# Optimization experiments

Hardware: AMD Instinct MI355X
Metric: run time of the kernel (lower is better)

The kernel has to match this reference:

```python
import jax, jax.numpy as jnp
import numpy as np

IN_DIMS = 256
EMBED_DIMS = 512
NUM_HEADS = 8
GRID = 16  # forced: arrange2 hardcodes 256 = GRID*GRID tokens
HEAD_DIM = EMBED_DIMS // NUM_HEADS
LN_EPS = 1e-5


def setup_inputs() -> dict:
    key = jax.random.key(0)
    ks = jax.random.split(key, 12)
    B = 8
    s_in = 1.0 / np.sqrt(IN_DIMS)
    s_emb = 1.0 / np.sqrt(EMBED_DIMS)
    return {
        "x1": jax.random.normal(ks[0], (B, IN_DIMS, GRID, GRID), jnp.float32),
        "x2": jax.random.normal(ks[1], (B, IN_DIMS, GRID, GRID), jnp.float32),
        # 1x1 conv weights stored as [out, in]
        "Wq": jax.random.normal(ks[2], (EMBED_DIMS, IN_DIMS), jnp.float32) * s_in,
        "bq": jnp.zeros((EMBED_DIMS,), jnp.float32),
        "Wk": jax.random.normal(ks[3], (EMBED_DIMS, IN_DIMS), jnp.float32) * s_in,
        "bk": jnp.zeros((EMBED_DIMS,), jnp.float32),
        "Wv": jax.random.normal(ks[4], (EMBED_DIMS, IN_DIMS), jnp.float32) * s_in,
        "bv": jnp.zeros((EMBED_DIMS,), jnp.float32),
        "Wa": jax.random.normal(ks[5], (IN_DIMS, EMBED_DIMS), jnp.float32) * s_emb,
        "ba": jnp.zeros((IN_DIMS,), jnp.float32),
        "ln_g": jnp.ones((IN_DIMS,), jnp.float32),
        "ln_b": jnp.zeros((IN_DIMS,), jnp.float32),
        "Wl": jax.random.normal(ks[6], (IN_DIMS, IN_DIMS), jnp.float32) * s_in,
        "bl": jnp.zeros((IN_DIMS,), jnp.float32),
    }


def _conv1x1(x, W, b):
    # x: [b, Cin, h, w]; W: [Cout, Cin]
    return jnp.einsum('bihw,oi->bohw', x, W) + b[None, :, None, None]


def _arrange(t):
    # 'b (c head) h w -> head b (h w) c'  (c outer, head inner in channel axis)
    b = t.shape[0]
    t = t.reshape(b, HEAD_DIM, NUM_HEADS, GRID * GRID)
    return t.transpose(2, 0, 3, 1)  # [head, b, n, c]


def reference(x1, x2, Wq, bq, Wk, bk, Wv, bv, Wa, ba, ln_g, ln_b, Wl, bl):
    B, Cin, H, W = x1.shape
    N = H * W  # 256
    q = _arrange(_conv1x1(x1, Wq, bq))                     # [h, b, n, c]
    k = _arrange(_conv1x1(x2, Wk, bk))                     # [h, q, m, c]
    v = _arrange(_conv1x1(x2, Wv, bv)).reshape(NUM_HEADS, B * N, HEAD_DIM)  # [h, (b m), c]
    # cross-batch attention logits (NOTE: original never applies self.scale)
    attn = jnp.einsum('pbnc,pqmc->pbqnm', q, k)            # [h, b, q, n, m]
    attn = jax.nn.softmax(attn, axis=-1)
    # 'head b q n m -> b head n (q m)'
    attn = attn.transpose(1, 0, 3, 2, 4).reshape(B, NUM_HEADS, N, B * N)
    out = jnp.einsum('bhnm,hmc->bhnc', attn, v)            # [b, h, n, c]
    # 'b head (h w) c -> b (c head) h w'
    out = out.transpose(0, 3, 1, 2).reshape(B, EMBED_DIMS, H, W)
    a = _conv1x1(out, Wa, ba) + x1                          # residual, [b, Cin, h, w]
    # proj_out: rearrange -> LayerNorm -> Linear -> ReLU -> rearrange back
    t = a.reshape(B, Cin, N).transpose(0, 2, 1)            # [b, n, Cin]
    mu = t.mean(-1, keepdims=True)
    var = ((t - mu) ** 2).mean(-1, keepdims=True)
    t = (t - mu) * jax.lax.rsqrt(var + LN_EPS) * ln_g + ln_b
    t = jax.nn.relu(t @ Wl.T + bl)
    return t.transpose(0, 2, 1).reshape(B, Cin, H, W)
```

## Files before the change

### kernel.cpp

```cpp
#include <hip/hip_runtime.h>

typedef unsigned short u16;
typedef unsigned int   u32;
typedef __attribute__((ext_vector_type(8))) short bf16x8;
typedef __attribute__((ext_vector_type(4))) float f32x4;

#define BB   8
#define CIN  256
#define NT   256
#define EMB  512
#define NH   8

__device__ __forceinline__ float bf2f(u16 b) {
    union { u32 u; float f; } v; v.u = ((u32)b) << 16; return v.f;
}
__device__ __forceinline__ u16 f2bf(float f) {
    union { float f; u32 u; } v; v.f = f;
    u32 r = v.u + 0x7FFFu + ((v.u >> 16) & 1u);
    return (u16)(r >> 16);
}
__device__ __forceinline__ float ld(const u16* base, size_t idx, int f32) {
    return f32 ? ((const float*)base)[idx] : bf2f(base[idx]);
}

struct alignas(16) U32x4 { u32 x, y, z, w; };
struct alignas(8)  U32x2 { u32 x, y; };

__global__ void k_xpose(
    const u16* __restrict__ x1, const u16* __restrict__ x2,
    const u16* __restrict__ Wq, const u16* __restrict__ Wk, const u16* __restrict__ Wv,
    u16* __restrict__ XTh, u16* __restrict__ XTl,
    u16* __restrict__ WCh, u16* __restrict__ WCl,
    int* __restrict__ flag)
{
    __shared__ int cnt;
    __shared__ float T[64][65];
    int t = threadIdx.x;
    if (t == 0) cnt = 0;
    __syncthreads();
    {
        int local = 0;
        for (int j = t * 16; j < t * 16 + 16; j += 2) {
            u16 w = x1[j];
            int e = (w >> 7) & 0xFF;
            if (e >= 100 && e <= 145) local++;
        }
        atomicAdd(&cnt, local);
    }
    __syncthreads();
    const int f32 = (cnt >= 1200) ? 0 : 1;

    int bid = blockIdx.x;
    if (bid == 0 && t == 0) *flag = f32;

    if (bid < 256) {
        int inp = bid >> 7, b = (bid >> 4) & 7, ks = (bid >> 2) & 3, ns = bid & 3;
        const u16* X = inp ? x2 : x1;
#pragma unroll
        for (int p = 0; p < 4; ++p) {
            int kk = p * 16 + (t >> 4);
            int nn = (t & 15) * 4;
#pragma unroll
            for (int j = 0; j < 4; ++j)
                T[kk][nn + j] = ld(X, ((size_t)b * CIN + ks * 64 + kk) * NT + ns * 64 + nn + j, f32);
        }
        __syncthreads();
#pragma unroll
        for (int it = 0; it < 2; ++it) {
            int g = it * 256 + t;
            int nn = g >> 3, kg = g & 7;
            u32 hw[4], lw[4];
#pragma unroll
            for (int e = 0; e < 4; ++e) {
                float va = T[kg * 8 + 2 * e][nn];
                float vb = T[kg * 8 + 2 * e + 1][nn];
                u16 ha = f2bf(va), hb = f2bf(vb);
                u16 la = f2bf(va - bf2f(ha)), lb = f2bf(vb - bf2f(hb));
                hw[e] = (u32)ha | ((u32)hb << 16);
                lw[e] = (u32)la | ((u32)lb << 16);
            }
            size_t dst = (((size_t)(inp * 8 + b) * 256) + ns * 64 + nn) * 256 + ks * 64 + kg * 8;
            U32x4 H; H.x = hw[0]; H.y = hw[1]; H.z = hw[2]; H.w = hw[3];
            U32x4 L; L.x = lw[0]; L.y = lw[1]; L.z = lw[2]; L.w = lw[3];
            *(U32x4*)&XTh[dst] = H;
            *(U32x4*)&XTl[dst] = L;
        }
    } else {
        int wb = bid - 256;
        int proj = wb >> 2, qtr = wb & 3;
        const u16* W = (proj == 0) ? Wq : (proj == 1) ? Wk : Wv;
#pragma unroll
        for (int it = 0; it < 16; ++it) {
            int g = it * 256 + t;
            int row = g >> 5, kg = g & 31;
            int o = qtr * 128 + row;
            u32 hw[4], lw[4];
#pragma unroll
            for (int e = 0; e < 4; ++e) {
                float va = ld(W, (size_t)o * CIN + kg * 8 + 2 * e, f32);
                float vb = ld(W, (size_t)o * CIN + kg * 8 + 2 * e + 1, f32);
                u16 ha = f2bf(va), hb = f2bf(vb);
                u16 la = f2bf(va - bf2f(ha)), lb = f2bf(vb - bf2f(hb));
                hw[e] = (u32)ha | ((u32)hb << 16);
                lw[e] = (u32)la | ((u32)lb << 16);
            }
            size_t dst = ((size_t)(proj * 512 + o)) * 256 + kg * 8;
            U32x4 H; H.x = hw[0]; H.y = hw[1]; H.z = hw[2]; H.w = hw[3];
            U32x4 L; L.x = lw[0]; L.y = lw[1]; L.z = lw[2]; L.w = lw[3];
            *(U32x4*)&WCh[dst] = H;
            *(U32x4*)&WCl[dst] = L;
        }
    }
}

__global__ __launch_bounds__(256) void k_qkv(
    const u16* __restrict__ XTh, const u16* __restrict__ XTl,
    const u16* __restrict__ WCh, const u16* __restrict__ WCl,
    const u16* __restrict__ bq, const u16* __restrict__ bk, const u16* __restrict__ bv,
    u16* __restrict__ Qg, u16* __restrict__ Kg, u16* __restrict__ Vg,
    const int* __restrict__ flag)
{
    const int f32 = *flag;
    int id = blockIdx.x;
    int proj = id >> 8;
    int rem  = id & 255;
    int b  = rem >> 5;
    int ot = (rem >> 2) & 7;
    int nt = rem & 3;

    __shared__ __align__(16) u16 SB[16384];
    const int WHO = 0, WLO = 4096, XHO = 8192, XLO = 12288;

    int t = threadIdx.x;
    int l = t & 63, w = t >> 6;
    int quad = l >> 4, col = l & 15;
    const int lswz2 = l ^ (((l >> 4) & 1) << 1);

    const u16* Wh  = WCh + ((size_t)proj * 512 + ot * 64) * 256;
    const u16* Wlo = WCl + ((size_t)proj * 512 + ot * 64) * 256;
    int inp = (proj == 0) ? 0 : 1;
    const u16* Xh  = XTh + (((size_t)(inp * 8 + b)) * 256 + nt * 64) * 256;
    const u16* Xlo = XTl + (((size_t)(inp * 8 + b)) * 256 + nt * 64) * 256;

    f32x4 acc[4];
#pragma unroll
    for (int n4 = 0; n4 < 4; ++n4) { acc[n4][0]=0.f; acc[n4][1]=0.f; acc[n4][2]=0.f; acc[n4][3]=0.f; }

    for (int c4 = 0; c4 < 4; ++c4) {
        __syncthreads();
#pragma unroll
        for (int it = 0; it < 2; ++it) {
            int g = it * 256 + t;
            int row = g >> 3, cc = g & 7;
            int tt = row >> 4, klo = row & 15, kch = cc >> 2, qs = cc & 3;
            int pos = qs * 16 + (klo ^ ((qs & 1) << 1) ^ (kch << 2));
            int off = ((tt * 2 + kch) * 64 + pos) * 8;
            size_t src = (size_t)row * 256 + c4 * 64 + cc * 8;
            *(U32x4*)&SB[WHO + off] = *(const U32x4*)&Wh[src];
            *(U32x4*)&SB[WLO + off] = *(const U32x4*)&Wlo[src];
            *(U32x4*)&SB[XHO + off] = *(const U32x4*)&Xh[src];
            *(U32x4*)&SB[XLO + off] = *(const U32x4*)&Xlo[src];
        }
        __syncthreads();

        int sA0 = ((w * 2 + 0) * 64 + lswz2) * 8;
        int sA1 = ((w * 2 + 1) * 64 + (lswz2 ^ 4)) * 8;
        bf16x8 aH0 = *(const bf16x8*)&SB[WHO + sA0];
        bf16x8 aH1 = *(const bf16x8*)&SB[WHO + sA1];
        bf16x8 aL0 = *(const bf16x8*)&SB[WLO + sA0];
        bf16x8 aL1 = *(const bf16x8*)&SB[WLO + sA1];
#pragma unroll
        for (int n4 = 0; n4 < 4; ++n4) {
            int sB0 = ((n4 * 2 + 0) * 64 + lswz2) * 8;
            int sB1 = ((n4 * 2 + 1) * 64 + (lswz2 ^ 4)) * 8;
            bf16x8 bH0 = *(const bf16x8*)&SB[XHO + sB0];
            bf16x8 bH1 = *(const bf16x8*)&SB[XHO + sB1];
            bf16x8 bL0 = *(const bf16x8*)&SB[XLO + sB0];
            bf16x8 bL1 = *(const bf16x8*)&SB[XLO + sB1];
            acc[n4] = __builtin_amdgcn_mfma_f32_16x16x32_bf16(aH0, bH0, acc[n4], 0, 0, 0);
            acc[n4] = __builtin_amdgcn_mfma_f32_16x16x32_bf16(aH1, bH1, acc[n4], 0, 0, 0);
            acc[n4] = __builtin_amdgcn_mfma_f32_16x16x32_bf16(aL0, bH0, acc[n4], 0, 0, 0);
            acc[n4] = __builtin_amdgcn_mfma_f32_16x16x32_bf16(aL1, bH1, acc[n4], 0, 0, 0);
            acc[n4] = __builtin_amdgcn_mfma_f32_16x16x32_bf16(aH0, bL0, acc[n4], 0, 0, 0);
            acc[n4] = __builtin_amdgcn_mfma_f32_16x16x32_bf16(aH1, bL1, acc[n4], 0, 0, 0);
        }
    }
    __syncthreads();

    float (*EP)[68] = (float (*)[68])SB;
    const u16* bias = (proj == 0) ? bq : (proj == 1) ? bk : bv;
#pragma unroll
    for (int r = 0; r < 4; ++r) {
        int ol = w * 16 + quad * 4 + r;
        float bb = ld(bias, ot * 64 + ol, f32);
#pragma unroll
        for (int n4 = 0; n4 < 4; ++n4)
            EP[ol][n4 * 16 + col] = acc[n4][r] + bb;
    }
    __syncthreads();

    if (proj < 2) {
        u16* OUT = (proj == 0) ? Qg : Kg;
        int hh = t >> 5;
        int nb = t & 31;
#pragma unroll
        for (int p = 0; p < 2; ++p) {
            int nn = nb + 32 * p;
            u32 pk[4];
#pragma unroll
            for (int e = 0; e < 4; ++e) {
                u16 lo = f2bf(EP[(2 * e) * 8 + hh][nn]);
                u16 hi = f2bf(EP[(2 * e + 1) * 8 + hh][nn]);
                pk[e] = (u32)lo | ((u32)hi << 16);
            }
            U32x4 v; v.x = pk[0]; v.y = pk[1]; v.z = pk[2]; v.w = pk[3];
            *(U32x4*)&OUT[((size_t)((hh * 8 + b) * 256) + nt * 64 + nn) * 64 + ot * 8] = v;
        }
    } else {
        int rr = t >> 2;
        int hh = rr & 7, cl = rr >> 3;
        int nq = t & 3;
        u32 pk[8];
#pragma unroll
        for (int e = 0; e < 8; ++e) {
            u16 lo = f2bf(EP[cl * 8 + hh][nq * 16 + 2 * e]);
            u16 hi = f2bf(EP[cl * 8 + hh][nq * 16 + 2 * e + 1]);
            pk[e] = (u32)lo | ((u32)hi << 16);
        }
        size_t base = ((size_t)((hh * 8 + b) * 64) + ot * 8 + cl) * 256 + nt * 64 + nq * 16;
        U32x4 v0; v0.x = pk[0]; v0.y = pk[1]; v0.z = pk[2]; v0.w = pk[3];
        U32x4 v1; v1.x = pk[4]; v1.y = pk[5]; v1.z = pk[6]; v1.w = pk[7];
        *(U32x4*)&Vg[base]     = v0;
        *(U32x4*)&Vg[base + 8] = v1;
    }
}

__device__ __forceinline__ void softmax_p(f32x4 (&Sfr)[16], bf16x8 (&pf)[8]) {
    float inv;
    {
        float m = Sfr[0][0];
#pragma unroll
        for (int tt = 0; tt < 16; ++tt)
#pragma unroll
            for (int r = 0; r < 4; ++r) m = fmaxf(m, Sfr[tt][r]);
        m = fmaxf(m, __shfl_xor(m, 16));
        m = fmaxf(m, __shfl_xor(m, 32));
        float s = 0.f;
#pragma unroll
        for (int tt = 0; tt < 16; ++tt)
#pragma unroll
            for (int r = 0; r < 4; ++r) {
                float e = __expf(Sfr[tt][r] - m);
                Sfr[tt][r] = e; s += e;
            }
        s += __shfl_xor(s, 16);
        s += __shfl_xor(s, 32);
        inv = 1.f / s;
    }
#pragma unroll
    for (int ch = 0; ch < 8; ++ch) {
        float a0 = Sfr[2*ch  ][0]*inv, a1 = Sfr[2*ch  ][1]*inv;
        float a2 = Sfr[2*ch  ][2]*inv, a3 = Sfr[2*ch  ][3]*inv;
        float b0 = Sfr[2*ch+1][0]*inv, b1 = Sfr[2*ch+1][1]*inv;
        float b2 = Sfr[2*ch+1][2]*inv, b3 = Sfr[2*ch+1][3]*inv;
        u32 u0, u1, v0, v1;
        asm("v_cvt_pk_bf16_f32 %0, %1, %2" : "=v"(u0) : "v"(a0), "v"(a1));
        asm("v_cvt_pk_bf16_f32 %0, %1, %2" : "=v"(u1) : "v"(a2), "v"(a3));
        asm("v_cvt_pk_bf16_f32 %0, %1, %2" : "=v"(v0) : "v"(b0), "v"(b1));
        asm("v_cvt_pk_bf16_f32 %0, %1, %2" : "=v"(v1) : "v"(b2), "v"(b3));
        asm("v_permlane32_swap_b32 %0, %1" : "+v"(u0), "+v"(v0));
        asm("v_permlane16_swap_b32 %0, %1" : "+v"(u0), "+v"(v0));
        asm("v_permlane32_swap_b32 %0, %1" : "+v"(u1), "+v"(v1));
        asm("v_permlane16_swap_b32 %0, %1" : "+v"(u1), "+v"(v1));
        union { u32 wd[4]; bf16x8 hB; } pu;
        pu.wd[0] = u0; pu.wd[1] = u1; pu.wd[2] = v0; pu.wd[3] = v1;
        pf[ch] = pu.hB;
    }
}

__global__ __launch_bounds__(256) void k_attn(
    const u16* __restrict__ Qg, const u16* __restrict__ Kg,
    const u16* __restrict__ Vg, float* __restrict__ Oph)
{
    int bid = blockIdx.x;
    int h      = bid & 7;
    int slot   = bid >> 3;
    int kbg    = slot >> 5;
    int member = slot & 31;
    int b      = member >> 2;
    int ntq    = member & 3;

    int t = threadIdx.x;
    int l = t & 63, w = t >> 6;
    int quad = l >> 4, col = l & 15;

    __shared__ __align__(16) u16 S[16384];

    int q = ntq*64 + w*16 + col;
    const size_t qrow = ((size_t)(h*8 + b)*256 + q)*64;
    bf16x8 qf0 = *(const bf16x8*)&Qg[qrow +  0 + quad*8];
    bf16x8 qf1 = *(const bf16x8*)&Qg[qrow + 32 + quad*8];

    const int lswz2 = l ^ (((l >> 4) & 1) << 1);
    const int lswz4 = l ^ (((l >> 4) & 1) << 2);

    f32x4 Oacc[4];
#pragma unroll
    for (int ct = 0; ct < 4; ++ct) { Oacc[ct][0]=0.f; Oacc[ct][1]=0.f; Oacc[ct][2]=0.f; Oacc[ct][3]=0.f; }

    for (int kb2 = 0; kb2 < 2; ++kb2) {
        int kb = kbg*2 + kb2;
        __syncthreads();
        const size_t kbase = (size_t)(h*8 + kb) * 256 * 64;
#pragma unroll
        for (int i = 0; i < 8; ++i) {
            int g = i*256 + t;
            int key = g >> 3, cc = g & 7;
            int tt = key >> 4, klo = key & 15, kc = cc >> 2, qs = cc & 3;
            int pos = qs*16 + (klo ^ ((qs & 1) << 1) ^ (kc << 2));
            U32x4 v = *(const U32x4*)&Kg[kbase + (size_t)key*64 + cc*8];
            *(U32x4*)&S[(size_t)(((tt*2 + kc)*64) + pos)*8] = v;
        }
        __syncthreads();

        f32x4 Sfr[16];
#pragma unroll
        for (int tt = 0; tt < 16; ++tt) { Sfr[tt][0]=0.f; Sfr[tt][1]=0.f; Sfr[tt][2]=0.f; Sfr[tt][3]=0.f; }
#pragma unroll
        for (int tt = 0; tt < 16; ++tt) {
            bf16x8 k0 = *(const bf16x8*)&S[(size_t)((tt*2 + 0)*64 + lswz2)*8];
            bf16x8 k1 = *(const bf16x8*)&S[(size_t)((tt*2 + 1)*64 + (lswz2 ^ 4))*8];
            Sfr[tt] = __builtin_amdgcn_mfma_f32_16x16x32_bf16(k0, qf0, Sfr[tt], 0, 0, 0);
            Sfr[tt] = __builtin_amdgcn_mfma_f32_16x16x32_bf16(k1, qf1, Sfr[tt], 0, 0, 0);
        }

        bf16x8 pf[8];
        softmax_p(Sfr, pf);
        __syncthreads();

        const size_t vbase = (size_t)(h*8 + kb) * 64 * 256;
#pragma unroll
        for (int i = 0; i < 8; ++i) {
            int g = i*256 + t;
            int cg = g >> 5, k16 = g & 31;
            int ct = cg >> 4, clo = cg & 15, ch = k16 >> 2, qs = k16 & 3;
            int pos = (qs*16 + clo) ^ ch ^ ((qs & 1) << 2);
            U32x4 v = *(const U32x4*)&Vg[vbase + (size_t)cg*256 + k16*8];
            *(U32x4*)&S[(size_t)(((ch*4 + ct)*64) + pos)*8] = v;
        }
        __syncthreads();

#pragma unroll
        for (int ch = 0; ch < 8; ++ch)
#pragma unroll
            for (int ct = 0; ct < 4; ++ct) {
                bf16x8 vb = *(const bf16x8*)&S[(size_t)(((ch*4 + ct)*64) + (lswz4 ^ ch))*8];
                Oacc[ct] = __builtin_amdgcn_mfma_f32_16x16x32_bf16(pf[ch], vb, Oacc[ct], 0, 0, 0);
            }
    }

    float* Op = Oph + (size_t)kbg * ((size_t)BB * EMB * NT);
    const size_t obase = (size_t)(h*8 + b) * 256 * 64;
    int n0 = ntq*64 + w*16 + quad*4;
#pragma unroll
    for (int ct = 0; ct < 4; ++ct)
#pragma unroll
        for (int r = 0; r < 4; ++r)
            Op[obase + (size_t)(n0 + r)*64 + ct*16 + col] = Oacc[ct][r];
}

__global__ __launch_bounds__(256) void k_proj_res(
    const float* __restrict__ Oph, const u16* __restrict__ Wa,
    const u16* __restrict__ ba, const u16* __restrict__ x1,
    float* __restrict__ Ap, const int* __restrict__ flag)
{
    const int f32 = *flag;
    int id = blockIdx.x;
    int it = id >> 6;
    int tt = id & 63;
    int tok0 = tt * 32;
    int b  = tok0 >> 8;
    int n0 = tok0 & 255;

    __shared__ float Was[64][68];
    __shared__ float Os[64][36];

    int t = threadIdx.x;
    int lane64 = t & 63, quad = t >> 6;
    int ig = t & 15;
    int tg = t >> 4;

    int tk = t & 31;
    int hh = t >> 5;

    const size_t SLAB = (size_t)BB * EMB * NT;

    float wreg[16];
    float oreg[8];

    {
#pragma unroll
        for (int p = 0; p < 16; ++p) {
            int i = quad + 4*p;
            wreg[p] = ld(Wa, (size_t)(it*64 + i)*EMB + 0*64 + lane64, f32);
        }
        const float* src = &Oph[(((size_t)(hh*8 + b))*256 + n0 + tk)*64 + 0*8];
#pragma unroll
        for (int s_ = 0; s_ < 4; ++s_) {
            const float* sp = src + (size_t)s_*SLAB;
            float4 v0 = *(const float4*)&sp[0];
            float4 v1 = *(const float4*)&sp[4];
            if (s_ == 0) {
                oreg[0]=v0.x; oreg[1]=v0.y; oreg[2]=v0.z; oreg[3]=v0.w;
                oreg[4]=v1.x; oreg[5]=v1.y; oreg[6]=v1.z; oreg[7]=v1.w;
            } else {
                oreg[0]+=v0.x; oreg[1]+=v0.y; oreg[2]+=v0.z; oreg[3]+=v0.w;
                oreg[4]+=v1.x; oreg[5]+=v1.y; oreg[6]+=v1.z; oreg[7]+=v1.w;
            }
        }
    }

    float acc[8];
#pragma unroll
    for (int j = 0; j < 8; ++j) acc[j] = 0.f;

    for (int kc = 0; kc < 8; ++kc) {
        __syncthreads();
#pragma unroll
        for (int p = 0; p < 16; ++p)
            Was[lane64][quad + 4*p] = wreg[p];
#pragma unroll
        for (int e = 0; e < 8; ++e)
            Os[e*8 + hh][tk] = oreg[e];
        __syncthreads();

        if (kc < 7) {
            int kn = kc + 1;
#pragma unroll
            for (int p = 0; p < 16; ++p) {
                int i = quad + 4*p;
                wreg[p] = ld(Wa, (size_t)(it*64 + i)*EMB + kn*64 + lane64, f32);
            }
            const float* src = &Oph[(((size_t)(hh*8 + b))*256 + n0 + tk)*64 + kn*8];
#pragma unroll
            for (int s_ = 0; s_ < 4; ++s_) {
                const float* sp = src + (size_t)s_*SLAB;
                float4 v0 = *(const float4*)&sp[0];
                float4 v1 = *(const float4*)&sp[4];
                if (s_ == 0) {
                    oreg[0]=v0.x; oreg[1]=v0.y; oreg[2]=v0.z; oreg[3]=v0.w;
                    oreg[4]=v1.x; oreg[5]=v1.y; oreg[6]=v1.z; oreg[7]=v1.w;
                } else {
                    oreg[0]+=v0.x; oreg[1]+=v0.y; oreg[2]+=v0.z; oreg[3]+=v0.w;
                    oreg[4]+=v1.x; oreg[5]+=v1.y; oreg[6]+=v1.z; oreg[7]+=v1.w;
                }
            }
        }

#pragma unroll 8
        for (int o = 0; o < 64; ++o) {
            float4 w4 = *(const float4*)&Was[o][ig*4];
            float2 t2 = *(const float2*)&Os[o][tg*2];
            acc[0] += w4.x*t2.x; acc[1] += w4.y*t2.x;
            acc[2] += w4.z*t2.x; acc[3] += w4.w*t2.x;
            acc[4] += w4.x*t2.y; acc[5] += w4.y*t2.y;
            acc[6] += w4.z*t2.y; acc[7] += w4.w*t2.y;
        }
    }

    int i0 = it*64 + ig*4;
    float ba0 = ld(ba, i0+0, f32), ba1 = ld(ba, i0+1, f32);
    float ba2 = ld(ba, i0+2, f32), ba3 = ld(ba, i0+3, f32);
#pragma unroll
    for (int jt = 0; jt < 2; ++jt) {
        int token = tok0 + tg*2 + jt;
        int n = n0 + tg*2 + jt;
        float4 v;
        v.x = acc[jt*4+0] + ba0 + ld(x1, ((size_t)b*CIN + i0+0)*NT + n, f32);
        v.y = acc[jt*4+1] + ba1 + ld(x1, ((size_t)b*CIN + i0+1)*NT + n, f32);
        v.z = acc[jt*4+2] + ba2 + ld(x1, ((size_t)b*CIN + i0+2)*NT + n, f32);
        v.w = acc[jt*4+3] + ba3 + ld(x1, ((size_t)b*CIN + i0+3)*NT + n, f32);
        *(float4*)&Ap[(size_t)token*CIN + i0] = v;
    }
}

__global__ void k_ln_out(
    const float* __restrict__ Ap, const u16* __restrict__ ln_g,
    const u16* __restrict__ ln_b, const u16* __restrict__ Wl,
    const u16* __restrict__ bl, u16* __restrict__ out,
    const int* __restrict__ flag)
{
    const int f32 = *flag;
    int tok0 = blockIdx.x * 8;
    int b  = tok0 >> 8;
    int n0 = tok0 & 255;

    __shared__ float At[8][260];

    int t = threadIdx.x;
#pragma unroll
    for (int k = 0; k < 8; ++k)
        At[k][t] = Ap[((size_t)tok0 + k)*CIN + t];
    __syncthreads();

    {
        int kk = t >> 5, lme = t & 31;
        float s = 0.f, s2 = 0.f;
#pragma unroll
        for (int ii = 0; ii < 8; ++ii) { float v = At[kk][lme + 32*ii]; s += v; s2 += v*v; }
#pragma unroll
        for (int off = 1; off < 32; off <<= 1) { s += __shfl_xor(s, off); s2 += __shfl_xor(s2, off); }
        float mu   = s  * (1.f/256.f);
        float var  = s2 * (1.f/256.f) - mu*mu;
        float rstd = rsqrtf(var + 1e-5f);
#pragma unroll
        for (int ii = 0; ii < 8; ++ii) {
            int i = lme + 32*ii;
            float v = At[kk][i];
            At[kk][i] = (v - mu) * rstd * ld(ln_g, i, f32) + ld(ln_b, i, f32);
        }
    }
    __syncthreads();

    int j = t;
    float acc[8];
#pragma unroll
    for (int k = 0; k < 8; ++k) acc[k] = 0.f;

    if (f32) {
        const float* wrow = (const float*)Wl + (size_t)j*CIN;
#pragma unroll 2
        for (int i4 = 0; i4 < 64; ++i4) {
            float4 w4 = *(const float4*)&wrow[4*i4];
#pragma unroll
            for (int k = 0; k < 8; ++k) {
                float4 a = *(const float4*)&At[k][4*i4];
                acc[k] += w4.x*a.x + w4.y*a.y + w4.z*a.z + w4.w*a.w;
            }
        }
    } else {
        const u32* wrow = (const u32*)(Wl + (size_t)j*CIN);
#pragma unroll 2
        for (int i4 = 0; i4 < 64; ++i4) {
            u32 w01 = wrow[2*i4+0], w23 = wrow[2*i4+1];
            float c0 = bf2f((u16)(w01 & 0xFFFFu)), c1 = bf2f((u16)(w01 >> 16));
            float c2 = bf2f((u16)(w23 & 0xFFFFu)), c3 = bf2f((u16)(w23 >> 16));
#pragma unroll
            for (int k = 0; k < 8; ++k) {
                float4 a = *(const float4*)&At[k][4*i4];
                acc[k] += c0*a.x + c1*a.y + c2*a.z + c3*a.w;
            }
        }
    }

    float blv = ld(bl, j, f32);
    size_t obase = ((size_t)b*CIN + j)*NT + n0;
    if (f32) {
        float* o32 = (float*)out;
#pragma unroll
        for (int k = 0; k < 8; ++k)
            o32[obase + k] = fmaxf(acc[k] + blv, 0.f);
    } else {
        u32 pk[4];
#pragma unroll
        for (int k = 0; k < 4; ++k) {
            float f0 = fmaxf(acc[2*k+0] + blv, 0.f);
            float f1 = fmaxf(acc[2*k+1] + blv, 0.f);
            pk[k] = (u32)f2bf(f0) | ((u32)f2bf(f1) << 16);
        }
        U32x4 a0; a0.x = pk[0]; a0.y = pk[1]; a0.z = pk[2]; a0.w = pk[3];
        *(U32x4*)(out + obase) = a0;
    }
}

extern "C" void kernel_launch(void* const* d_in, const int* in_sizes, int n_in,
                              void* d_out, int out_size, void* d_ws, size_t ws_size,
                              hipStream_t stream)
{
    const u16* x1   = (const u16*)d_in[0];
    const u16* x2   = (const u16*)d_in[1];
    const u16* Wq   = (const u16*)d_in[2];
    const u16* bq   = (const u16*)d_in[3];
    const u16* Wk   = (const u16*)d_in[4];
    const u16* bk   = (const u16*)d_in[5];
    const u16* Wv   = (const u16*)d_in[6];
    const u16* bv   = (const u16*)d_in[7];
    const u16* Wa   = (const u16*)d_in[8];
    const u16* ba   = (const u16*)d_in[9];
    const u16* ln_g = (const u16*)d_in[10];
    const u16* ln_b = (const u16*)d_in[11];
    const u16* Wl   = (const u16*)d_in[12];
    const u16* bl   = (const u16*)d_in[13];
    u16* out = (u16*)d_out;

    int* flag = (int*)d_ws;
    u16* Qg = (u16*)d_ws + 32;
    u16* Kg = Qg + (size_t)BB*EMB*NT;
    u16* Vg = Kg + (size_t)BB*EMB*NT;
    float* Oph = (float*)(Vg + (size_t)BB*EMB*NT);
    float* Ap  = Oph + 4*(size_t)BB*EMB*NT;
    u16* XTh = (u16*)(Ap + (size_t)BB*NT*CIN);
    u16* XTl = XTh + (size_t)2*BB*NT*CIN;
    u16* WCh = XTl + (size_t)2*BB*NT*CIN;
    u16* WCl = WCh + (size_t)3*EMB*CIN;

    k_xpose   <<<268,  256, 0, stream>>>(x1, x2, Wq, Wk, Wv, XTh, XTl, WCh, WCl, flag);
    k_qkv     <<<768,  256, 0, stream>>>(XTh, XTl, WCh, WCl, bq, bk, bv, Qg, Kg, Vg, flag);
    k_attn    <<<1024, 256, 0, stream>>>(Qg, Kg, Vg, Oph);
    k_proj_res<<<256,  256, 0, stream>>>(Oph, Wa, ba, x1, Ap, flag);
    k_ln_out  <<<256,  256, 0, stream>>>(Ap, ln_g, ln_b, Wl, bl, out, flag);
}
```

Measured before the change: 188.3 us.

## Halve attention split-K partials and prefetch K/V tiles into registers

The attention kernel now handles four key batches per block instead of two, which halves the grid to 512 blocks and halves the number of fp32 partial-output slabs. The projection kernel therefore sums two slabs instead of four. Inside the attention loop, K for the next batch and V for the current batch are loaded from global memory into registers ahead of time, so the loads overlap with the QK MFMAs and the softmax. The cost is higher register pressure, fewer blocks for latency hiding, and a longer serial loop per block.

```diff
diff --git a/kernel.cpp b/kernel.cpp
--- a/kernel.cpp
+++ b/kernel.cpp
@@ -308,18 +308,35 @@
 #pragma unroll
     for (int ct = 0; ct < 4; ++ct) { Oacc[ct][0]=0.f; Oacc[ct][1]=0.f; Oacc[ct][2]=0.f; Oacc[ct][3]=0.f; }
 
-    for (int kb2 = 0; kb2 < 2; ++kb2) {
-        int kb = kbg*2 + kb2;
-        __syncthreads();
-        const size_t kbase = (size_t)(h*8 + kb) * 256 * 64;
+    U32x4 kreg[8], vreg[8];
+
+    {
+        const size_t kbase = (size_t)(h*8 + kbg*4) * 256 * 64;
+#pragma unroll
+        for (int i = 0; i < 8; ++i) {
+            int g = i*256 + t;
+            kreg[i] = *(const U32x4*)&Kg[kbase + (size_t)(g >> 3)*64 + (g & 7)*8];
+        }
+    }
+
+    for (int kb2 = 0; kb2 < 4; ++kb2) {
+        int kb = kbg*4 + kb2;
+        __syncthreads();
 #pragma unroll
         for (int i = 0; i < 8; ++i) {
             int g = i*256 + t;
             int key = g >> 3, cc = g & 7;
             int tt = key >> 4, klo = key & 15, kc = cc >> 2, qs = cc & 3;
             int pos = qs*16 + (klo ^ ((qs & 1) << 1) ^ (kc << 2));
-            U32x4 v = *(const U32x4*)&Kg[kbase + (size_t)key*64 + cc*8];
-            *(U32x4*)&S[(size_t)(((tt*2 + kc)*64) + pos)*8] = v;
+            *(U32x4*)&S[(size_t)(((tt*2 + kc)*64) + pos)*8] = kreg[i];
+        }
+        {
+            const size_t vbase = (size_t)(h*8 + kb) * 64 * 256;
+#pragma unroll
+            for (int i = 0; i < 8; ++i) {
+                int g = i*256 + t;
+                vreg[i] = *(const U32x4*)&Vg[vbase + (size_t)(g >> 5)*256 + (g & 31)*8];
+            }
         }
         __syncthreads();
 
@@ -334,19 +351,26 @@
             Sfr[tt] = __builtin_amdgcn_mfma_f32_16x16x32_bf16(k1, qf1, Sfr[tt], 0, 0, 0);
         }
 
+        if (kb2 < 3) {
+            const size_t kbase = (size_t)(h*8 + kb + 1) * 256 * 64;
+#pragma unroll
+            for (int i = 0; i < 8; ++i) {
+                int g = i*256 + t;
+                kreg[i] = *(const U32x4*)&Kg[kbase + (size_t)(g >> 3)*64 + (g & 7)*8];
+            }
+        }
+
         bf16x8 pf[8];
         softmax_p(Sfr, pf);
         __syncthreads();
 
-        const size_t vbase = (size_t)(h*8 + kb) * 64 * 256;
 #pragma unroll
         for (int i = 0; i < 8; ++i) {
             int g = i*256 + t;
             int cg = g >> 5, k16 = g & 31;
             int ct = cg >> 4, clo = cg & 15, ch = k16 >> 2, qs = k16 & 3;
             int pos = (qs*16 + clo) ^ ch ^ ((qs & 1) << 2);
-            U32x4 v = *(const U32x4*)&Vg[vbase + (size_t)cg*256 + k16*8];
-            *(U32x4*)&S[(size_t)(((ch*4 + ct)*64) + pos)*8] = v;
+            *(U32x4*)&S[(size_t)(((ch*4 + ct)*64) + pos)*8] = vreg[i];
         }
         __syncthreads();
 
@@ -405,19 +429,12 @@
             wreg[p] = ld(Wa, (size_t)(it*64 + i)*EMB + 0*64 + lane64, f32);
         }
         const float* src = &Oph[(((size_t)(hh*8 + b))*256 + n0 + tk)*64 + 0*8];
-#pragma unroll
-        for (int s_ = 0; s_ < 4; ++s_) {
-            const float* sp = src + (size_t)s_*SLAB;
-            float4 v0 = *(const float4*)&sp[0];
-            float4 v1 = *(const float4*)&sp[4];
-            if (s_ == 0) {
-                oreg[0]=v0.x; oreg[1]=v0.y; oreg[2]=v0.z; oreg[3]=v0.w;
-                oreg[4]=v1.x; oreg[5]=v1.y; oreg[6]=v1.z; oreg[7]=v1.w;
-            } else {
-                oreg[0]+=v0.x; oreg[1]+=v0.y; oreg[2]+=v0.z; oreg[3]+=v0.w;
-                oreg[4]+=v1.x; oreg[5]+=v1.y; oreg[6]+=v1.z; oreg[7]+=v1.w;
-            }
-        }
+        float4 v0 = *(const float4*)&src[0];
+        float4 v1 = *(const float4*)&src[4];
+        float4 u0 = *(const float4*)&src[SLAB];
+        float4 u1 = *(const float4*)&src[SLAB + 4];
+        oreg[0]=v0.x+u0.x; oreg[1]=v0.y+u0.y; oreg[2]=v0.z+u0.z; oreg[3]=v0.w+u0.w;
+        oreg[4]=v1.x+u1.x; oreg[5]=v1.y+u1.y; oreg[6]=v1.z+u1.z; oreg[7]=v1.w+u1.w;
     }
 
     float acc[8];
@@ -442,19 +459,12 @@
                 wreg[p] = ld(Wa, (size_t)(it*64 + i)*EMB + kn*64 + lane64, f32);
             }
             const float* src = &Oph[(((size_t)(hh*8 + b))*256 + n0 + tk)*64 + kn*8];
-#pragma unroll
-            for (int s_ = 0; s_ < 4; ++s_) {
-                const float* sp = src + (size_t)s_*SLAB;
-                float4 v0 = *(const float4*)&sp[0];
-                float4 v1 = *(const float4*)&sp[4];
-                if (s_ == 0) {
-                    oreg[0]=v0.x; oreg[1]=v0.y; oreg[2]=v0.z; oreg[3]=v0.w;
-                    oreg[4]=v1.x; oreg[5]=v1.y; oreg[6]=v1.z; oreg[7]=v1.w;
-                } else {
-                    oreg[0]+=v0.x; oreg[1]+=v0.y; oreg[2]+=v0.z; oreg[3]+=v0.w;
-                    oreg[4]+=v1.x; oreg[5]+=v1.y; oreg[6]+=v1.z; oreg[7]+=v1.w;
-                }
-            }
+            float4 v0 = *(const float4*)&src[0];
+            float4 v1 = *(const float4*)&src[4];
+            float4 u0 = *(const float4*)&src[SLAB];
+            float4 u1 = *(const float4*)&src[SLAB + 4];
+            oreg[0]=v0.x+u0.x; oreg[1]=v0.y+u0.y; oreg[2]=v0.z+u0.z; oreg[3]=v0.w+u0.w;
+            oreg[4]=v1.x+u1.x; oreg[5]=v1.y+u1.y; oreg[6]=v1.z+u1.z; oreg[7]=v1.w+u1.w;
         }
 
 #pragma unroll 8
@@ -604,9 +614,9 @@
     u16* WCh = XTl + (size_t)2*BB*NT*CIN;
     u16* WCl = WCh + (size_t)3*EMB*CIN;
 
-    k_xpose   <<<268,  256, 0, stream>>>(x1, x2, Wq, Wk, Wv, XTh, XTl, WCh, WCl, flag);
-    k_qkv     <<<768,  256, 0, stream>>>(XTh, XTl, WCh, WCl, bq, bk, bv, Qg, Kg, Vg, flag);
-    k_attn    <<<1024, 256, 0, stream>>>(Qg, Kg, Vg, Oph);
-    k_proj_res<<<256,  256, 0, stream>>>(Oph, Wa, ba, x1, Ap, flag);
-    k_ln_out  <<<256,  256, 0, stream>>>(Ap, ln_g, ln_b, Wl, bl, out, flag);
-}
+    k_xpose   <<<268, 256, 0, stream>>>(x1, x2, Wq, Wk, Wv, XTh, XTl, WCh, WCl, flag);
+    k_qkv     <<<768, 256, 0, stream>>>(XTh, XTl, WCh, WCl, bq, bk, bv, Qg, Kg, Vg, flag);
+    k_attn    <<<512, 256, 0, stream>>>(Qg, Kg, Vg, Oph);
+    k_proj_res<<<256, 256, 0, stream>>>(Oph, Wa, ba, x1, Ap, flag);
+    k_ln_out  <<<256, 256, 0, stream>>>(Ap, ln_g, ln_b, Wl, bl, out, flag);
+}
```

Result: slower. 217.7 us (+15.6%).
